# Kernel tuning notes

Hardware: AMD Instinct MI355X
Metric: run time of the kernel (lower is better)

## Reference

```python
import jax, jax.numpy as jnp
import numpy as np

EPS = 1e-6
ENERGY_THRESHOLD = 0.95
LS_INIT = 1e-5


def setup_inputs() -> dict:
    key = jax.random.key(0)
    k_x, k_u, k_s, k_v = jax.random.split(key, 4)
    dim, max_rank = 4096, 16
    x = jax.random.normal(k_x, (4, 2048, dim), dtype=jnp.float32)
    U = jax.random.normal(k_u, (dim, max_rank), dtype=jnp.float32) * 0.02
    S = jax.random.uniform(k_s, (max_rank,), dtype=jnp.float32)
    V = jax.random.normal(k_v, (max_rank, dim), dtype=jnp.float32) * 0.02
    norm_weight = jnp.ones((dim,), dtype=jnp.float32)
    gamma = jnp.full((dim,), LS_INIT, dtype=jnp.float32)
    return {"x": x, "U": U, "S": S, "V": V,
            "norm_weight": norm_weight, "gamma": gamma}


def _rank_mask(S):
    # Effective rank from singular-value energy (non-differentiable decision,
    # matching torch's .item() host sync which detaches it from autograd).
    s_abs = jnp.abs(S)
    cum = jnp.cumsum(s_abs) / jnp.maximum(s_abs.sum(), 1e-8)
    hit = cum >= ENERGY_THRESHOLD
    r = jnp.where(hit.any(), jnp.argmax(hit) + 1, S.shape[0])
    keep = (jnp.arange(S.shape[0]) < r).astype(S.dtype)
    return jax.lax.stop_gradient(keep)


def reference(x, U, S, V, norm_weight, gamma):
    # RMSNorm (computed in fp32, matching x.float() in torch)
    xf = x.astype(jnp.float32)
    x_norm = (xf * jax.lax.rsqrt(jnp.mean(xf * xf, axis=-1, keepdims=True) + EPS)).astype(x.dtype)
    x_norm = x_norm * norm_weight
    # Adaptive-rank low-rank projection: masking columns >= r equals slicing [:r]
    keep = _rank_mask(S)
    h = jnp.einsum('bsd,dr->bsr', x_norm, U)        # [B,S,max_rank]
    h = h * (S * keep)                               # zero out ranks >= r
    h = jnp.einsum('bsr,rd->bsd', h, V)             # [B,S,dim]
    # LayerScale + residual
    return x + h * gamma
```

## Files before the change

kernel.cpp:

```cpp
#include <hip/hip_runtime.h>

#define DIM   4096
#define RANK  16
#define BM    16
#define NT    512
#define NWAVE 8
#define NST   8

typedef __fp16 f16;
typedef __fp16 half4 __attribute__((ext_vector_type(4)));
typedef __fp16 half8 __attribute__((ext_vector_type(8)));
typedef float  floatx4 __attribute__((ext_vector_type(4)));

#define VM_WAIT(N) { asm volatile("s_waitcnt vmcnt(" #N ")" ::: "memory"); \
                     __builtin_amdgcn_sched_barrier(0); }
#define SCHED_FENCE() __builtin_amdgcn_sched_barrier(0)

__device__ __forceinline__ void gld16(const void* g, void* l) {
    __builtin_amdgcn_global_load_lds((__attribute__((address_space(1))) void*)g,
                                     (__attribute__((address_space(3))) void*)l,
                                     16, 0, 0);
}

__global__ __launch_bounds__(256) void prep_weights(const float* __restrict__ U,
    const float* __restrict__ nw, const float* __restrict__ V,
    f16* __restrict__ Ub, f16* __restrict__ Vb)
{
    const int i   = blockIdx.x * 256 + threadIdx.x;
    const int l   = i & 63;
    const int n   = l & 15;
    const int blk = l >> 4;
    if (i < 8192) {
        const int kb = i >> 6;
        half8 u;
        #pragma unroll
        for (int e = 0; e < 8; ++e) {
            const int k = kb * 32 + blk * 8 + e;
            u[e] = (f16)(nw[k] * U[(size_t)k * RANK + n]);
        }
        *(half8*)(Ub + (size_t)i * 8) = u;
    }
    {
        const int cb = i >> 6;
        half4 v;
        #pragma unroll
        for (int e = 0; e < 4; ++e) {
            const int k = blk * 4 + e;
            v[e] = (f16)V[(size_t)k * DIM + cb * 16 + n];
        }
        *(half4*)(Vb + (size_t)i * 4) = v;
    }
}

__global__ __launch_bounds__(NT, 4) void arl_fused(
    const float* __restrict__ x,  const f16* __restrict__ Ub,
    const f16* __restrict__ Vb,   const float* __restrict__ S,
    const float* __restrict__ gamma, float* __restrict__ out)
{
    const int t   = threadIdx.x;
    const int w   = t >> 6;
    const int l   = t & 63;
    const int n   = l & 15;
    const int blk = l >> 4;
    const size_t row0 = (size_t)blockIdx.x * BM;

    __shared__ __align__(16) float ring[NWAVE][2][BM * 64];
    __shared__ float s_hacc[NWAVE][16][17];
    __shared__ float s_ssq[NWAVE][16];
    __shared__ __align__(8) f16 s_hh[16][16];

    const float* xg = x + row0 * DIM + w * 512;

    floatx4 acc = {0.f, 0.f, 0.f, 0.f};
    float ssq = 0.f;

    #pragma unroll
    for (int j = 0; j < 4; ++j) {
        const int rl  = 4 * j + (l >> 4);
        const int gsw = (l & 15) ^ (rl & 7);
        gld16(xg + (size_t)rl * DIM + gsw * 4, &ring[w][0][j * 256]);
    }

    #pragma unroll 1
    for (int st = 0; st < NST; ++st) {
        const int kb0 = w * 16 + st * 2;
        const half8 ub0 = *(const half8*)(Ub + ((size_t)kb0 * 64 + l) * 8);
        const half8 ub1 = *(const half8*)(Ub + ((size_t)(kb0 + 1) * 64 + l) * 8);
        SCHED_FENCE();
        if (st + 1 < NST) {
            #pragma unroll
            for (int j = 0; j < 4; ++j) {
                const int rl  = 4 * j + (l >> 4);
                const int gsw = (l & 15) ^ (rl & 7);
                gld16(xg + (size_t)rl * DIM + (st + 1) * 64 + gsw * 4,
                      &ring[w][(st + 1) & 1][j * 256]);
            }
            VM_WAIT(6)
        } else {
            VM_WAIT(2)
        }

        const float* buf = ring[w][st & 1];
        #pragma unroll
        for (int s = 0; s < 2; ++s) {
            const int g0 = (s * 8 + blk * 2)     ^ (n & 7);
            const int g1 = (s * 8 + blk * 2 + 1) ^ (n & 7);
            const float4 xa0 = *(const float4*)&buf[n * 64 + g0 * 4];
            const float4 xa1 = *(const float4*)&buf[n * 64 + g1 * 4];
            ssq = fmaf(xa0.x, xa0.x, ssq); ssq = fmaf(xa0.y, xa0.y, ssq);
            ssq = fmaf(xa0.z, xa0.z, ssq); ssq = fmaf(xa0.w, xa0.w, ssq);
            ssq = fmaf(xa1.x, xa1.x, ssq); ssq = fmaf(xa1.y, xa1.y, ssq);
            ssq = fmaf(xa1.z, xa1.z, ssq); ssq = fmaf(xa1.w, xa1.w, ssq);
            half8 a;
            a[0] = (f16)xa0.x; a[1] = (f16)xa0.y; a[2] = (f16)xa0.z; a[3] = (f16)xa0.w;
            a[4] = (f16)xa1.x; a[5] = (f16)xa1.y; a[6] = (f16)xa1.z; a[7] = (f16)xa1.w;
            acc = __builtin_amdgcn_mfma_f32_16x16x32_f16(a, s ? ub1 : ub0, acc, 0, 0, 0);
        }
    }

    ssq += __shfl_xor(ssq, 16, 64);
    ssq += __shfl_xor(ssq, 32, 64);
    if (l < 16) s_ssq[w][l] = ssq;

    #pragma unroll
    for (int j = 0; j < 4; ++j) s_hacc[w][blk * 4 + j][n] = acc[j];
    __syncthreads();

    if (t < 256) {
        const int m = t >> 4, q = t & 15;
        float hsum = 0.f, tssq = 0.f;
        #pragma unroll
        for (int ww = 0; ww < NWAVE; ++ww) {
            hsum += s_hacc[ww][m][q];
            tssq += s_ssq[ww][m];
        }
        const float rstd = rsqrtf(tssq * (1.0f / DIM) + 1e-6f);
        float tot = 0.f;
        #pragma unroll
        for (int i = 0; i < RANK; ++i) tot += fabsf(S[i]);
        const float denom = fmaxf(tot, 1e-8f);
        float cum = 0.f, se = 0.f;
        #pragma unroll
        for (int i = 0; i < RANK; ++i) {
            if (i == q) se = ((cum / denom) < 0.95f) ? S[i] : 0.f;
            cum += fabsf(S[i]);
        }
        s_hh[m][q] = (f16)(hsum * se * rstd);
    }
    __syncthreads();

    const half4 ah = *(const half4*)&s_hh[n][blk * 4];
    const half4* Vb4 = (const half4*)Vb;
    const floatx4 zero = {0.f, 0.f, 0.f, 0.f};
    const float* xrow = x   + (row0 + n) * DIM;
    float*       orow = out + (row0 + n) * DIM;

    #pragma unroll 4
    for (int i = 0; i < 32; ++i) {
        const int cb = w * 32 + i;
        const int c0 = cb * 16 + blk * 4;
        const half4 bv = Vb4[(size_t)cb * 64 + l];
        floatx4 d = __builtin_amdgcn_mfma_f32_16x16x16f16(bv, ah, zero, 0, 0, 0);
        const float4 g  = *(const float4*)(gamma + c0);
        const float4 xv = *(const float4*)(xrow + c0);
        floatx4 o;
        o[0] = fmaf(g.x, d[0], xv.x);
        o[1] = fmaf(g.y, d[1], xv.y);
        o[2] = fmaf(g.z, d[2], xv.z);
        o[3] = fmaf(g.w, d[3], xv.w);
        __builtin_nontemporal_store(o, (floatx4*)(orow + c0));
    }
}

extern "C" void kernel_launch(void* const* d_in, const int* in_sizes, int n_in,
                              void* d_out, int out_size, void* d_ws, size_t ws_size,
                              hipStream_t stream) {
    (void)in_sizes; (void)n_in; (void)ws_size;
    const float* x  = (const float*)d_in[0];
    const float* U  = (const float*)d_in[1];
    const float* S  = (const float*)d_in[2];
    const float* V  = (const float*)d_in[3];
    const float* nw = (const float*)d_in[4];
    const float* g  = (const float*)d_in[5];
    float* out = (float*)d_out;
    f16* Ub = (f16*)d_ws;
    f16* Vb = (f16*)((char*)d_ws + 128 * 1024);

    hipLaunchKernelGGL(prep_weights, dim3(64), dim3(256), 0, stream,
                       U, nw, V, Ub, Vb);

    const int rows = out_size / DIM;
    const int grid = rows / BM;
    hipLaunchKernelGGL(arl_fused, dim3(grid), dim3(NT), 0, stream,
                       x, Ub, Vb, S, g, out);
}
```

Baseline: 74.65 us.

## Warp-specialize fused kernel into producer and consumer waves over two row tiles

New measurement: 74.90 us. About the same (+0.3%).

```diff
diff --git a/kernel.cpp b/kernel.cpp
--- a/kernel.cpp
+++ b/kernel.cpp
@@ -3,8 +3,9 @@
 #define DIM   4096
 #define RANK  16
 #define BM    16
-#define NT    512
-#define NWAVE 8
+#define NT    1024
+#define NAW   8
+#define TPB   2
 #define NST   8
 
 typedef __fp16 f16;
@@ -62,113 +63,147 @@
     const int l   = t & 63;
     const int n   = l & 15;
     const int blk = l >> 4;
-    const size_t row0 = (size_t)blockIdx.x * BM;
-
-    __shared__ __align__(16) float ring[NWAVE][2][BM * 64];
-    __shared__ float s_hacc[NWAVE][16][17];
-    __shared__ float s_ssq[NWAVE][16];
-    __shared__ __align__(8) f16 s_hh[16][16];
-
-    const float* xg = x + row0 * DIM + w * 512;
-
-    floatx4 acc = {0.f, 0.f, 0.f, 0.f};
-    float ssq = 0.f;
-
-    #pragma unroll
-    for (int j = 0; j < 4; ++j) {
-        const int rl  = 4 * j + (l >> 4);
-        const int gsw = (l & 15) ^ (rl & 7);
-        gld16(xg + (size_t)rl * DIM + gsw * 4, &ring[w][0][j * 256]);
-    }
-
-    #pragma unroll 1
-    for (int st = 0; st < NST; ++st) {
-        const int kb0 = w * 16 + st * 2;
-        const half8 ub0 = *(const half8*)(Ub + ((size_t)kb0 * 64 + l) * 8);
-        const half8 ub1 = *(const half8*)(Ub + ((size_t)(kb0 + 1) * 64 + l) * 8);
-        SCHED_FENCE();
-        if (st + 1 < NST) {
+    const size_t rowB = (size_t)blockIdx.x * (BM * TPB);
+
+    __shared__ __align__(16) float ring[NAW][2][BM * 64];
+    __shared__ float s_hacc[TPB][NAW][16][17];
+    __shared__ float s_ssq[TPB][NAW][16];
+    __shared__ __align__(8) f16 s_hh[TPB][16][16];
+    __shared__ int s_cnt[TPB];
+    __shared__ int s_flag[TPB];
+
+    if (t == 0) { s_cnt[0] = 0; s_cnt[1] = 0; s_flag[0] = 0; s_flag[1] = 0; }
+    __syncthreads();
+
+    if (w < NAW) {
+        floatx4 acc = {0.f, 0.f, 0.f, 0.f};
+        float ssq = 0.f;
+
+        #pragma unroll
+        for (int j = 0; j < 4; ++j) {
+            const int rl  = 4 * j + (l >> 4);
+            const int gsw = (l & 15) ^ (rl & 7);
+            gld16(x + (rowB + rl) * DIM + (size_t)w * 512 + gsw * 4,
+                  &ring[w][0][j * 256]);
+        }
+
+        #pragma unroll 1
+        for (int g = 0; g < TPB * NST; ++g) {
+            const int st = g & (NST - 1);
+            const int kb0 = w * 16 + st * 2;
+            const half8 ub0 = *(const half8*)(Ub + ((size_t)kb0 * 64 + l) * 8);
+            const half8 ub1 = *(const half8*)(Ub + ((size_t)(kb0 + 1) * 64 + l) * 8);
+            SCHED_FENCE();
+            if (g + 1 < TPB * NST) {
+                const int tn = (g + 1) >> 3, sn = (g + 1) & (NST - 1);
+                #pragma unroll
+                for (int j = 0; j < 4; ++j) {
+                    const int rl  = 4 * j + (l >> 4);
+                    const int gsw = (l & 15) ^ (rl & 7);
+                    gld16(x + (rowB + tn * BM + rl) * DIM + (size_t)w * 512
+                            + (size_t)sn * 64 + gsw * 4,
+                          &ring[w][(g + 1) & 1][j * 256]);
+                }
+                VM_WAIT(6)
+            } else {
+                VM_WAIT(2)
+            }
+
+            const float* buf = ring[w][g & 1];
             #pragma unroll
-            for (int j = 0; j < 4; ++j) {
-                const int rl  = 4 * j + (l >> 4);
-                const int gsw = (l & 15) ^ (rl & 7);
-                gld16(xg + (size_t)rl * DIM + (st + 1) * 64 + gsw * 4,
-                      &ring[w][(st + 1) & 1][j * 256]);
-            }
-            VM_WAIT(6)
-        } else {
-            VM_WAIT(2)
-        }
-
-        const float* buf = ring[w][st & 1];
-        #pragma unroll
-        for (int s = 0; s < 2; ++s) {
-            const int g0 = (s * 8 + blk * 2)     ^ (n & 7);
-            const int g1 = (s * 8 + blk * 2 + 1) ^ (n & 7);
-            const float4 xa0 = *(const float4*)&buf[n * 64 + g0 * 4];
-            const float4 xa1 = *(const float4*)&buf[n * 64 + g1 * 4];
-            ssq = fmaf(xa0.x, xa0.x, ssq); ssq = fmaf(xa0.y, xa0.y, ssq);
-            ssq = fmaf(xa0.z, xa0.z, ssq); ssq = fmaf(xa0.w, xa0.w, ssq);
-            ssq = fmaf(xa1.x, xa1.x, ssq); ssq = fmaf(xa1.y, xa1.y, ssq);
-            ssq = fmaf(xa1.z, xa1.z, ssq); ssq = fmaf(xa1.w, xa1.w, ssq);
-            half8 a;
-            a[0] = (f16)xa0.x; a[1] = (f16)xa0.y; a[2] = (f16)xa0.z; a[3] = (f16)xa0.w;
-            a[4] = (f16)xa1.x; a[5] = (f16)xa1.y; a[6] = (f16)xa1.z; a[7] = (f16)xa1.w;
-            acc = __builtin_amdgcn_mfma_f32_16x16x32_f16(a, s ? ub1 : ub0, acc, 0, 0, 0);
-        }
-    }
-
-    ssq += __shfl_xor(ssq, 16, 64);
-    ssq += __shfl_xor(ssq, 32, 64);
-    if (l < 16) s_ssq[w][l] = ssq;
-
-    #pragma unroll
-    for (int j = 0; j < 4; ++j) s_hacc[w][blk * 4 + j][n] = acc[j];
-    __syncthreads();
-
-    if (t < 256) {
-        const int m = t >> 4, q = t & 15;
-        float hsum = 0.f, tssq = 0.f;
-        #pragma unroll
-        for (int ww = 0; ww < NWAVE; ++ww) {
-            hsum += s_hacc[ww][m][q];
-            tssq += s_ssq[ww][m];
-        }
-        const float rstd = rsqrtf(tssq * (1.0f / DIM) + 1e-6f);
-        float tot = 0.f;
-        #pragma unroll
-        for (int i = 0; i < RANK; ++i) tot += fabsf(S[i]);
-        const float denom = fmaxf(tot, 1e-8f);
-        float cum = 0.f, se = 0.f;
-        #pragma unroll
-        for (int i = 0; i < RANK; ++i) {
-            if (i == q) se = ((cum / denom) < 0.95f) ? S[i] : 0.f;
-            cum += fabsf(S[i]);
-        }
-        s_hh[m][q] = (f16)(hsum * se * rstd);
-    }
-    __syncthreads();
-
-    const half4 ah = *(const half4*)&s_hh[n][blk * 4];
-    const half4* Vb4 = (const half4*)Vb;
-    const floatx4 zero = {0.f, 0.f, 0.f, 0.f};
-    const float* xrow = x   + (row0 + n) * DIM;
-    float*       orow = out + (row0 + n) * DIM;
-
-    #pragma unroll 4
-    for (int i = 0; i < 32; ++i) {
-        const int cb = w * 32 + i;
-        const int c0 = cb * 16 + blk * 4;
-        const half4 bv = Vb4[(size_t)cb * 64 + l];
-        floatx4 d = __builtin_amdgcn_mfma_f32_16x16x16f16(bv, ah, zero, 0, 0, 0);
-        const float4 g  = *(const float4*)(gamma + c0);
-        const float4 xv = *(const float4*)(xrow + c0);
-        floatx4 o;
-        o[0] = fmaf(g.x, d[0], xv.x);
-        o[1] = fmaf(g.y, d[1], xv.y);
-        o[2] = fmaf(g.z, d[2], xv.z);
-        o[3] = fmaf(g.w, d[3], xv.w);
-        __builtin_nontemporal_store(o, (floatx4*)(orow + c0));
+            for (int s = 0; s < 2; ++s) {
+                const int g0 = (s * 8 + blk * 2)     ^ (n & 7);
+                const int g1 = (s * 8 + blk * 2 + 1) ^ (n & 7);
+                const float4 xa0 = *(const float4*)&buf[n * 64 + g0 * 4];
+                const float4 xa1 = *(const float4*)&buf[n * 64 + g1 * 4];
+                ssq = fmaf(xa0.x, xa0.x, ssq); ssq = fmaf(xa0.y, xa0.y, ssq);
+                ssq = fmaf(xa0.z, xa0.z, ssq); ssq = fmaf(xa0.w, xa0.w, ssq);
+                ssq = fmaf(xa1.x, xa1.x, ssq); ssq = fmaf(xa1.y, xa1.y, ssq);
+                ssq = fmaf(xa1.z, xa1.z, ssq); ssq = fmaf(xa1.w, xa1.w, ssq);
+                half8 a;
+                a[0] = (f16)xa0.x; a[1] = (f16)xa0.y; a[2] = (f16)xa0.z; a[3] = (f16)xa0.w;
+                a[4] = (f16)xa1.x; a[5] = (f16)xa1.y; a[6] = (f16)xa1.z; a[7] = (f16)xa1.w;
+                acc = __builtin_amdgcn_mfma_f32_16x16x32_f16(a, s ? ub1 : ub0, acc, 0, 0, 0);
+            }
+
+            if (st == NST - 1) {
+                const int ti = g >> 3;
+                float sq = ssq;
+                sq += __shfl_xor(sq, 16, 64);
+                sq += __shfl_xor(sq, 32, 64);
+                if (l < 16) s_ssq[ti][w][l] = sq;
+                #pragma unroll
+                for (int j = 0; j < 4; ++j) s_hacc[ti][w][blk * 4 + j][n] = acc[j];
+                __threadfence_block();
+                int r = 0;
+                if (l == 0) r = atomicAdd(&s_cnt[ti], 1);
+                r = __shfl(r, 0, 64);
+                if (r == NAW - 1) {
+                    float tot = 0.f;
+                    #pragma unroll
+                    for (int i = 0; i < RANK; ++i) tot += fabsf(S[i]);
+                    const float denom = fmaxf(tot, 1e-8f);
+                    #pragma unroll
+                    for (int j = 0; j < 4; ++j) {
+                        const int p = l * 4 + j;
+                        const int m = p >> 4, q = p & 15;
+                        float hsum = 0.f, tssq = 0.f;
+                        #pragma unroll
+                        for (int ww = 0; ww < NAW; ++ww) {
+                            hsum += s_hacc[ti][ww][m][q];
+                            tssq += s_ssq[ti][ww][m];
+                        }
+                        const float rstd = rsqrtf(tssq * (1.0f / DIM) + 1e-6f);
+                        float cum = 0.f, se = 0.f;
+                        #pragma unroll
+                        for (int i = 0; i < RANK; ++i) {
+                            if (i == q) se = ((cum / denom) < 0.95f) ? S[i] : 0.f;
+                            cum += fabsf(S[i]);
+                        }
+                        s_hh[ti][m][q] = (f16)(hsum * se * rstd);
+                    }
+                    __threadfence_block();
+                    if (l == 0) atomicExch(&s_flag[ti], 1);
+                }
+                acc[0] = 0.f; acc[1] = 0.f; acc[2] = 0.f; acc[3] = 0.f;
+                ssq = 0.f;
+            }
+        }
+    } else {
+        const int wb = w - NAW;
+        const half4* Vb4 = (const half4*)Vb;
+        const floatx4 zero = {0.f, 0.f, 0.f, 0.f};
+
+        #pragma unroll 1
+        for (int ti = 0; ti < TPB; ++ti) {
+            int ready = 0;
+            while (!ready) {
+                if (l == 0) ready = atomicAdd(&s_flag[ti], 0);
+                ready = __shfl(ready, 0, 64);
+                if (!ready) __builtin_amdgcn_s_sleep(8);
+            }
+
+            const half4 ah = *(const half4*)&s_hh[ti][n][blk * 4];
+            const size_t row0 = rowB + (size_t)ti * BM;
+            const float* xrow = x   + (row0 + n) * DIM;
+            float*       orow = out + (row0 + n) * DIM;
+
+            #pragma unroll 4
+            for (int i = 0; i < 32; ++i) {
+                const int cb = wb * 32 + i;
+                const int c0 = cb * 16 + blk * 4;
+                const half4 bv = Vb4[(size_t)cb * 64 + l];
+                floatx4 d = __builtin_amdgcn_mfma_f32_16x16x16f16(bv, ah, zero, 0, 0, 0);
+                const float4 g  = *(const float4*)(gamma + c0);
+                const float4 xv = *(const float4*)(xrow + c0);
+                floatx4 o;
+                o[0] = fmaf(g.x, d[0], xv.x);
+                o[1] = fmaf(g.y, d[1], xv.y);
+                o[2] = fmaf(g.z, d[2], xv.z);
+                o[3] = fmaf(g.w, d[3], xv.w);
+                __builtin_nontemporal_store(o, (floatx4*)(orow + c0));
+            }
+        }
     }
 }
 
@@ -190,7 +225,7 @@
                        U, nw, V, Ub, Vb);
 
     const int rows = out_size / DIM;
-    const int grid = rows / BM;
+    const int grid = rows / (BM * TPB);
     hipLaunchKernelGGL(arl_fused, dim3(grid), dim3(NT), 0, stream,
                        x, Ub, Vb, S, g, out);
 }
```
